# Kernel tuning notes

Measured on AMD Instinct MI355X. Metric: run time of the kernel, lower is better.

The kernel has to match this reference:

```python
import jax, jax.numpy as jnp
import numpy as np

B, L, D = 8, 2048, 512
H, P = 8, 4
C = D // H  # dim_per_head


def setup_inputs() -> dict:
    key = jax.random.key(0)
    ks = jax.random.split(key, 11)
    sc = lambda k, shape, s=0.02: jax.random.normal(k, shape, jnp.float32) * s
    return dict(
        query=jax.random.normal(ks[0], (B, L, D), jnp.float32),
        key_in=jax.random.normal(ks[1], (B, L, D), jnp.float32),
        value=jax.random.normal(ks[2], (B, L, D), jnp.float32),
        W_v=sc(ks[3], (D, D)), b_v=jnp.zeros((D,), jnp.float32),
        W_off=sc(ks[4], (D, H * P * 2), 0.01), b_off=sc(ks[5], (H * P * 2,), 0.2),
        W_aw=sc(ks[6], (D, H * P), 0.01), b_aw=jnp.zeros((H * P,), jnp.float32),
        W_out=sc(ks[7], (D, D)), b_out=jnp.zeros((D,), jnp.float32),
    )


def reference(query, key_in, value, W_v, b_v, W_off, b_off, W_aw, b_aw, W_out, b_out):
    # value projection
    v = value @ W_v + b_v                                        # (B,L,D)
    # sampling offsets and attention weights from the query
    off = (query @ W_off + b_off).reshape(B, L, H, P, 2)         # (B,L,H,P,2)
    aw = jax.nn.softmax((query @ W_aw + b_aw).reshape(B, L, H, P), axis=-1)
    # reference point for query i is (x=linspace[0]=0, y=linspace[i]) because
    # the torch code slices reference_points[:, :, :, :1, :]
    ref_y = jnp.linspace(0.0, 1.0, L, dtype=jnp.float32)
    loc_x = jnp.clip(off[..., 0], 0.0, 1.0)                      # ref_x = 0
    loc_y = jnp.clip(off[..., 1] + ref_y[None, :, None, None], 0.0, 1.0)
    # grid_sample, align_corners=False, input (BH, C, 1, L)
    ix = ((loc_x + 1.0) * L - 1.0) * 0.5                         # width coord in [ (L-1)/2, L-0.5 ]
    iy = loc_y * 0.5                                             # ((y+1)*1 - 1)/2
    ix0 = jnp.floor(ix)
    fx = ix - ix0
    iy0 = jnp.floor(iy)
    fy = iy - iy0
    # height dim has size 1: row iy0 valid iff ==0, row iy0+1 valid iff ==0 (zero padding)
    ywt = (1.0 - fy) * (iy0 == 0.0).astype(jnp.float32) + fy * ((iy0 + 1.0) == 0.0).astype(jnp.float32)
    i0 = ix0.astype(jnp.int32)
    i1 = i0 + 1

    perm = lambda a: a.transpose(0, 2, 1, 3)                     # (B,L,H,P) -> (B,H,L,P)
    i0p, i1p = perm(i0), perm(i1)
    vh = v.reshape(B, L, H, C).transpose(0, 2, 1, 3)             # (B,H,L,C)

    gather = jax.vmap(jax.vmap(lambda vm, ii: vm[ii]))           # (L,C),(L,P) -> (L,P,C)
    m0 = ((i0p >= 0) & (i0p < L)).astype(jnp.float32)[..., None]
    m1 = ((i1p >= 0) & (i1p < L)).astype(jnp.float32)[..., None]
    g0 = gather(vh, jnp.clip(i0p, 0, L - 1)) * m0                # (B,H,L,P,C)
    g1 = gather(vh, jnp.clip(i1p, 0, L - 1)) * m1

    fxp = perm(fx)[..., None]
    ywtp = perm(ywt)[..., None]
    samp = ywtp * ((1.0 - fxp) * g0 + fxp * g1)                  # (B,H,L,P,C)
    out = (samp * perm(aw)[..., None]).sum(axis=3)               # (B,H,L,C)
    out = out.transpose(0, 2, 1, 3).reshape(B, L, D)
    return out @ W_out + b_out
```

## Files before the change

### kernel.cpp

```cpp
#include <hip/hip_runtime.h>
#include <stdint.h>

#define PSZF (16384 * 96)

using short8  = __attribute__((ext_vector_type(8))) short;
using floatx4 = __attribute__((ext_vector_type(4))) float;

__device__ __forceinline__ unsigned short f2bf(float f) {
  union { float f; unsigned u; } v; v.f = f;
  unsigned r = v.u + 0x7fffu + ((v.u >> 16) & 1u);
  return (unsigned short)(r >> 16);
}
__device__ __forceinline__ float bf2f(unsigned short u) {
  union { unsigned u; float f; } v; v.u = ((unsigned)u) << 16; return v.f;
}

__device__ __forceinline__ void load_lds16(const void* g, void* l) {
  __builtin_amdgcn_global_load_lds(
      (const __attribute__((address_space(1))) unsigned int*)g,
      (__attribute__((address_space(3))) unsigned int*)l, 16, 0, 0);
}

__device__ __forceinline__ void store_val(float* p, float v) { *p = v; }
__device__ __forceinline__ void store_val(unsigned short* p, float v) { *p = f2bf(v); }

__global__ __launch_bounds__(256) void prep_all(const float* __restrict__ value,
                                                const float* __restrict__ W_v,
                                                const float* __restrict__ W_out,
                                                const float* __restrict__ Woff,
                                                const float* __restrict__ Waw,
                                                const float* __restrict__ boff,
                                                const float* __restrict__ baw,
                                                unsigned short* __restrict__ val_bf,
                                                unsigned short* __restrict__ Wv_t,
                                                unsigned short* __restrict__ Wo_t,
                                                unsigned short* __restrict__ Bhi,
                                                unsigned short* __restrict__ Blo,
                                                float* __restrict__ bcat) {
  int idx = blockIdx.x * 256 + threadIdx.x;
  if (idx < 2097152) {
    float4 v = ((const float4*)value)[idx];
    ushort4 o;
    o.x = f2bf(v.x); o.y = f2bf(v.y); o.z = f2bf(v.z); o.w = f2bf(v.w);
    ((ushort4*)val_bf)[idx] = o;
    return;
  }
  int t = idx - 2097152;
  if (t < 262144) {
    int n = t >> 9, k = t & 511;
    Wv_t[t] = f2bf(W_v[(k << 9) + n]);
    return;
  }
  t -= 262144;
  if (t < 262144) {
    int n = t >> 9, k = t & 511;
    Wo_t[t] = f2bf(W_out[(k << 9) + n]);
    return;
  }
  t -= 262144;
  if (t < 49152) {
    int n = t >> 9, k = t & 511;
    float w = (n < 64) ? Woff[(k << 6) + n] : Waw[(k << 5) + (n - 64)];
    unsigned short hi = f2bf(w);
    Bhi[t] = hi;
    Blo[t] = f2bf(w - bf2f(hi));
    return;
  }
  t -= 49152;
  if (t < 96) bcat[t] = (t < 64) ? boff[t] : baw[t - 64];
}

template <typename OutT>
__device__ __forceinline__ void gemm_body64(unsigned char* smem,
                                            const unsigned short* __restrict__ A,
                                            const unsigned short* __restrict__ Bt,
                                            const float* __restrict__ bias,
                                            OutT* __restrict__ C, int bx, int by) {
  unsigned short* lA = (unsigned short*)smem;
  unsigned short* lB = (unsigned short*)(smem + 16384);
  int tid  = threadIdx.x;
  int lane = tid & 63, wv = tid >> 6;
  int wm = wv & 1, wn = wv >> 1;
  int lrow = lane & 15, quad = lane >> 4;
  int rowBlk = by * 128, colBlk = bx * 128;

  const unsigned short* Ab = A + (size_t)rowBlk * 512;
  const unsigned short* Bb = Bt + (size_t)colBlk * 512;
  int r0 = tid >> 2;
  int c0 = (tid & 3) << 3;

  floatx4 acc[4][4];
#pragma unroll
  for (int i = 0; i < 4; i++)
#pragma unroll
    for (int j = 0; j < 4; j++) acc[i][j] = (floatx4){0.f, 0.f, 0.f, 0.f};

  for (int k0 = 0; k0 < 512; k0 += 64) {
    load_lds16(Ab + (size_t)r0 * 512 + k0 + c0,             lA + tid * 8);
    load_lds16(Ab + (size_t)(r0 + 64) * 512 + k0 + c0,      lA + 2048 + tid * 8);
    load_lds16(Bb + (size_t)r0 * 512 + k0 + c0,             lB + tid * 8);
    load_lds16(Bb + (size_t)(r0 + 64) * 512 + k0 + c0,      lB + 2048 + tid * 8);
    load_lds16(Ab + (size_t)r0 * 512 + k0 + 32 + c0,        lA + 4096 + tid * 8);
    load_lds16(Ab + (size_t)(r0 + 64) * 512 + k0 + 32 + c0, lA + 6144 + tid * 8);
    load_lds16(Bb + (size_t)r0 * 512 + k0 + 32 + c0,        lB + 4096 + tid * 8);
    load_lds16(Bb + (size_t)(r0 + 64) * 512 + k0 + 32 + c0, lB + 6144 + tid * 8);
    __syncthreads();

#pragma unroll
    for (int kc = 0; kc < 2; kc++) {
      short8 a[4], b[4];
#pragma unroll
      for (int mi = 0; mi < 4; mi++)
        a[mi] = *(const short8*)&lA[kc * 4096 + (wm * 64 + mi * 16 + lrow) * 32 + quad * 8];
#pragma unroll
      for (int ni = 0; ni < 4; ni++)
        b[ni] = *(const short8*)&lB[kc * 4096 + (wn * 64 + ni * 16 + lrow) * 32 + quad * 8];
#pragma unroll
      for (int mi = 0; mi < 4; mi++)
#pragma unroll
        for (int ni = 0; ni < 4; ni++)
          acc[mi][ni] = __builtin_amdgcn_mfma_f32_16x16x32_bf16(a[mi], b[ni], acc[mi][ni], 0, 0, 0);
    }
    __syncthreads();
  }

#pragma unroll
  for (int ni = 0; ni < 4; ni++) {
    int col = colBlk + wn * 64 + ni * 16 + lrow;
    float bv = bias[col];
#pragma unroll
    for (int mi = 0; mi < 4; mi++) {
      int row = rowBlk + wm * 64 + mi * 16 + quad * 4;
#pragma unroll
      for (int r = 0; r < 4; r++)
        store_val(&C[(size_t)(row + r) * 512 + col], acc[mi][ni][r] + bv);
    }
  }
}

__device__ __forceinline__ void swz512(int bid, int& bx, int& by) {
  int x = bid & 7, s = bid >> 3;
  by = (x << 4) | (s >> 2);
  bx = s & 3;
}

__device__ __forceinline__ void offaw_body(unsigned char* smem,
                                           const float* __restrict__ Q,
                                           const unsigned short* __restrict__ Bhi,
                                           const unsigned short* __restrict__ Blo,
                                           const float* __restrict__ bcat,
                                           float* __restrict__ P, int bid) {
  unsigned short* lAhi = (unsigned short*)smem;
  unsigned short* lAlo = (unsigned short*)(smem + 4096);
  unsigned short* lBhi = (unsigned short*)(smem + 8192);
  unsigned short* lBlo = (unsigned short*)(smem + 14336);
  int khalf = bid >> 8, row0 = (bid & 255) * 64, kbase = khalf << 8;
  int tid = threadIdx.x, lane = tid & 63, wv = tid >> 6;
  int wm = wv & 1, wn = wv >> 1, lrow = lane & 15, quad = lane >> 4;

  int ar = tid >> 2, ac = (tid & 3) << 3;
  const float* qp = Q + (size_t)(row0 + ar) * 512 + kbase + ac;

  floatx4 acc[2][3];
#pragma unroll
  for (int i = 0; i < 2; i++)
#pragma unroll
    for (int j = 0; j < 3; j++) acc[i][j] = (floatx4){0.f, 0.f, 0.f, 0.f};

  for (int k0 = 0; k0 < 256; k0 += 32) {
    float4 v0 = *(const float4*)(qp + k0);
    float4 v1 = *(const float4*)(qp + k0 + 4);
    float vv[8] = {v0.x, v0.y, v0.z, v0.w, v1.x, v1.y, v1.z, v1.w};
    short8 h8, l8;
#pragma unroll
    for (int e = 0; e < 8; e++) {
      union { float f; unsigned u; } t; t.f = vv[e];
      unsigned r = t.u + 0x7fffu + ((t.u >> 16) & 1u);
      h8[e] = (short)(r >> 16);
      union { unsigned u; float f; } hf; hf.u = r & 0xffff0000u;
      union { float f; unsigned u; } rb; rb.f = vv[e] - hf.f;
      l8[e] = (short)(rb.u >> 16);
    }
    *(short8*)&lAhi[tid * 8] = h8;
    *(short8*)&lAlo[tid * 8] = l8;
#pragma unroll
    for (int j = 0; j < 3; j++) {
      int widx = wv + (j << 2);
      const unsigned short* src = (widx < 6) ? Bhi : Blo;
      unsigned short* dst = (widx < 6) ? lBhi : lBlo;
      int c = (((widx < 6) ? widx : widx - 6) << 6) + lane;
      int n = c >> 2, cc = (c & 3) << 3;
      load_lds16(src + (size_t)n * 512 + kbase + k0 + cc, dst + c * 8);
    }
    __syncthreads();

    short8 ah[2], al[2], bh[3], bl[3];
#pragma unroll
    for (int mi = 0; mi < 2; mi++) {
      int r = (wm * 32 + mi * 16 + lrow) * 32 + quad * 8;
      ah[mi] = *(const short8*)&lAhi[r];
      al[mi] = *(const short8*)&lAlo[r];
    }
#pragma unroll
    for (int ni = 0; ni < 3; ni++) {
      int r = (wn * 48 + ni * 16 + lrow) * 32 + quad * 8;
      bh[ni] = *(const short8*)&lBhi[r];
      bl[ni] = *(const short8*)&lBlo[r];
    }
#pragma unroll
    for (int mi = 0; mi < 2; mi++)
#pragma unroll
      for (int ni = 0; ni < 3; ni++) {
        acc[mi][ni] = __builtin_amdgcn_mfma_f32_16x16x32_bf16(ah[mi], bh[ni], acc[mi][ni], 0, 0, 0);
        acc[mi][ni] = __builtin_amdgcn_mfma_f32_16x16x32_bf16(ah[mi], bl[ni], acc[mi][ni], 0, 0, 0);
        acc[mi][ni] = __builtin_amdgcn_mfma_f32_16x16x32_bf16(al[mi], bh[ni], acc[mi][ni], 0, 0, 0);
      }
    __syncthreads();
  }

  float* out = P + (size_t)khalf * PSZF;
#pragma unroll
  for (int ni = 0; ni < 3; ni++) {
    int col = wn * 48 + ni * 16 + lrow;
    float bv = (khalf == 0) ? bcat[col] : 0.0f;
#pragma unroll
    for (int mi = 0; mi < 2; mi++) {
      int row = row0 + wm * 32 + mi * 16 + quad * 4;
#pragma unroll
      for (int r = 0; r < 4; r++)
        out[(size_t)(row + r) * 96 + col] = acc[mi][ni][r] + bv;
    }
  }
}

__global__ __launch_bounds__(256) void mega_k1(const unsigned short* __restrict__ val_bf,
                                               const unsigned short* __restrict__ Wv_t,
                                               const float* __restrict__ b_v,
                                               unsigned short* __restrict__ v_bf,
                                               const float* __restrict__ query,
                                               const unsigned short* __restrict__ Bhi,
                                               const unsigned short* __restrict__ Blo,
                                               const float* __restrict__ bcat,
                                               float* __restrict__ offP) {
  __shared__ __align__(16) unsigned char smem[32768];
  int bid = blockIdx.x;
  if (bid < 512) {
    int bx, by; swz512(bid, bx, by);
    gemm_body64<unsigned short>(smem, val_bf, Wv_t, b_v, v_bf, bx, by);
  } else {
    offaw_body(smem, query, Bhi, Blo, bcat, offP, bid - 512);
  }
}

__global__ __launch_bounds__(256) void gemm2_k(const unsigned short* __restrict__ A,
                                               const unsigned short* __restrict__ Bt,
                                               const float* __restrict__ bias,
                                               float* __restrict__ C) {
  __shared__ __align__(16) unsigned char smem[32768];
  int bx, by; swz512(blockIdx.x, bx, by);
  gemm_body64<float>(smem, A, Bt, bias, C, bx, by);
}

__global__ __launch_bounds__(256) void sample_kernel(const float* __restrict__ P,
                                                     const unsigned short* __restrict__ v,
                                                     unsigned short* __restrict__ attn) {
  int tid = threadIdx.x;
  int rr = tid >> 5, hp = tid & 31;
  int row = blockIdx.x * 8 + rr;
  int l = row & 2047;
  __shared__ float s_w0[8][32], s_w1[8][32];
  __shared__ int s_i0[8][32], s_i1[8][32];
  {
    int base = row * 96;
    float lg = P[base + 64 + hp] + P[PSZF + base + 64 + hp];
    float mx = fmaxf(lg, __shfl_xor(lg, 1));
    mx = fmaxf(mx, __shfl_xor(mx, 2));
    float e = __expf(lg - mx);
    float s = e + __shfl_xor(e, 1);
    s = s + __shfl_xor(s, 2);
    float aw = e / s;

    float ox = P[base + 2 * hp] + P[PSZF + base + 2 * hp];
    float oy = P[base + 2 * hp + 1] + P[PSZF + base + 2 * hp + 1];
    float refy = (float)l * (1.0f / 2047.0f);
    float lx = fminf(fmaxf(ox, 0.0f), 1.0f);
    float ly = fminf(fmaxf(oy + refy, 0.0f), 1.0f);
    float ix = ((lx + 1.0f) * 2048.0f - 1.0f) * 0.5f;
    float ywt = 1.0f - ly * 0.5f;
    float ix0 = floorf(ix);
    float fx = ix - ix0;
    int i0 = (int)ix0;
    int i1 = i0 + 1;
    s_w0[rr][hp] = aw * ywt * (1.0f - fx);
    s_w1[rr][hp] = (i1 < 2048) ? (aw * ywt * fx) : 0.0f;
    s_i0[rr][hp] = i0;
    s_i1[rr][hp] = (i1 < 2048) ? i1 : 2047;
  }
  __syncthreads();

  int b = (blockIdx.x * 8) >> 11;
  int h = tid >> 5, c = (tid & 31) << 1;
  const unsigned short* vhc = v + ((size_t)(b << 11)) * 512 + h * 64 + c;
#pragma unroll
  for (int r8 = 0; r8 < 8; r8++) {
    int row2 = blockIdx.x * 8 + r8;
    float ax = 0.0f, ay = 0.0f;
#pragma unroll
    for (int p = 0; p < 4; p++) {
      int t = (h << 2) + p;
      unsigned g0 = *(const unsigned*)(vhc + ((size_t)s_i0[r8][t] << 9));
      unsigned g1 = *(const unsigned*)(vhc + ((size_t)s_i1[r8][t] << 9));
      float w0 = s_w0[r8][t], w1 = s_w1[r8][t];
      ax += w0 * bf2f((unsigned short)g0) + w1 * bf2f((unsigned short)g1);
      ay += w0 * bf2f((unsigned short)(g0 >> 16)) + w1 * bf2f((unsigned short)(g1 >> 16));
    }
    unsigned packed = (unsigned)f2bf(ax) | ((unsigned)f2bf(ay) << 16);
    *(unsigned*)(attn + (size_t)row2 * 512 + h * 64 + c) = packed;
  }
}

extern "C" void kernel_launch(void* const* d_in, const int* in_sizes, int n_in,
                              void* d_out, int out_size, void* d_ws, size_t ws_size,
                              hipStream_t stream) {
  (void)in_sizes; (void)n_in; (void)out_size; (void)ws_size;
  const float* query = (const float*)d_in[0];
  const float* value = (const float*)d_in[2];
  const float* W_v   = (const float*)d_in[3];
  const float* b_v   = (const float*)d_in[4];
  const float* W_off = (const float*)d_in[5];
  const float* b_off = (const float*)d_in[6];
  const float* W_aw  = (const float*)d_in[7];
  const float* b_aw  = (const float*)d_in[8];
  const float* W_out = (const float*)d_in[9];
  const float* b_out = (const float*)d_in[10];
  float* out = (float*)d_out;

  char* ws = (char*)d_ws;
  const size_t MB = 1ull << 20;
  unsigned short* val_bf = (unsigned short*)(ws);
  unsigned short* attn   = val_bf;
  unsigned short* v_bf   = (unsigned short*)(ws + 16 * MB);
  float* offP            = (float*)(ws + 32 * MB);
  unsigned short* Wv_t   = (unsigned short*)(ws + 48 * MB);
  unsigned short* Wo_t   = (unsigned short*)(ws + 48 * MB + 524288);
  unsigned short* Bhi    = (unsigned short*)(ws + 49 * MB);
  unsigned short* Blo    = (unsigned short*)(ws + 49 * MB + 98304);
  float* bcat            = (float*)(ws + 49 * MB + 196608);

  prep_all<<<10433, 256, 0, stream>>>(value, W_v, W_out, W_off, W_aw, b_off, b_aw,
                                      val_bf, Wv_t, Wo_t, Bhi, Blo, bcat);
  mega_k1<<<1024, 256, 0, stream>>>(val_bf, Wv_t, b_v, v_bf, query, Bhi, Blo, bcat, offP);
  sample_kernel<<<2048, 256, 0, stream>>>(offP, v_bf, attn);
  gemm2_k<<<512, 256, 0, stream>>>(attn, Wo_t, b_out, out);
}
```

Before: 192.7 us.

## Fuse deformable sampling with output projection GEMM via LDS-staged tile

Merges the sampling kernel and the output-projection GEMM into one kernel. Each block computes a 32-row bf16 attention tile in shared memory, then multiplies it by W_out with MFMA, reading the B operand straight from global memory. This drops the global round trip of the attention intermediate and one launch. In exchange there are only 512 blocks, each using about 48KB of shared memory, and W_out is re-read per block without LDS staging, so occupancy and B-operand bandwidth may suffer.

Measured after the change: 227.6 us. +18.1%, slower.

```diff
diff --git a/kernel.cpp b/kernel.cpp
--- a/kernel.cpp
+++ b/kernel.cpp
@@ -252,25 +252,26 @@
   }
 }
 
-__global__ __launch_bounds__(256) void gemm2_k(const unsigned short* __restrict__ A,
-                                               const unsigned short* __restrict__ Bt,
-                                               const float* __restrict__ bias,
-                                               float* __restrict__ C) {
-  __shared__ __align__(16) unsigned char smem[32768];
-  int bx, by; swz512(blockIdx.x, bx, by);
-  gemm_body64<float>(smem, A, Bt, bias, C, bx, by);
-}
-
-__global__ __launch_bounds__(256) void sample_kernel(const float* __restrict__ P,
-                                                     const unsigned short* __restrict__ v,
-                                                     unsigned short* __restrict__ attn) {
+__global__ __launch_bounds__(256) void sample_out_kernel(const float* __restrict__ P,
+                                                         const unsigned short* __restrict__ v,
+                                                         const unsigned short* __restrict__ Wo,
+                                                         const float* __restrict__ bias,
+                                                         float* __restrict__ out) {
+  __shared__ float s_w0[32][32], s_w1[32][32];
+  __shared__ int s_i0[32][32], s_i1[32][32];
+  __shared__ __align__(16) unsigned short s_attn[16384];
+
   int tid = threadIdx.x;
+  int bid = blockIdx.x;
+  int sw = ((bid & 7) << 6) + (bid >> 3);
+  int row0 = sw << 5;
+
   int rr = tid >> 5, hp = tid & 31;
-  int row = blockIdx.x * 8 + rr;
-  int l = row & 2047;
-  __shared__ float s_w0[8][32], s_w1[8][32];
-  __shared__ int s_i0[8][32], s_i1[8][32];
-  {
+#pragma unroll
+  for (int it = 0; it < 4; ++it) {
+    int rl = (it << 3) + rr;
+    int row = row0 + rl;
+    int l = row & 2047;
     int base = row * 96;
     float lg = P[base + 64 + hp] + P[PSZF + base + 64 + hp];
     float mx = fmaxf(lg, __shfl_xor(lg, 1));
@@ -291,22 +292,23 @@
     float fx = ix - ix0;
     int i0 = (int)ix0;
     int i1 = i0 + 1;
-    s_w0[rr][hp] = aw * ywt * (1.0f - fx);
-    s_w1[rr][hp] = (i1 < 2048) ? (aw * ywt * fx) : 0.0f;
-    s_i0[rr][hp] = i0;
-    s_i1[rr][hp] = (i1 < 2048) ? i1 : 2047;
+    s_w0[rl][hp] = aw * ywt * (1.0f - fx);
+    s_w1[rl][hp] = (i1 < 2048) ? (aw * ywt * fx) : 0.0f;
+    s_i0[rl][hp] = i0;
+    s_i1[rl][hp] = (i1 < 2048) ? i1 : 2047;
   }
   __syncthreads();
 
-  int b = (blockIdx.x * 8) >> 11;
+  int b = row0 >> 11;
   int h = tid >> 5, c = (tid & 31) << 1;
   const unsigned short* vhc = v + ((size_t)(b << 11)) * 512 + h * 64 + c;
-#pragma unroll
-  for (int r8 = 0; r8 < 8; r8++) {
-    int row2 = blockIdx.x * 8 + r8;
+  int ch = h * 64 + c;
+  char* sa = (char*)s_attn + ((ch >> 5) << 11) + ((c & 31) << 1);
+#pragma unroll 4
+  for (int r8 = 0; r8 < 32; ++r8) {
     float ax = 0.0f, ay = 0.0f;
 #pragma unroll
-    for (int p = 0; p < 4; p++) {
+    for (int p = 0; p < 4; ++p) {
       int t = (h << 2) + p;
       unsigned g0 = *(const unsigned*)(vhc + ((size_t)s_i0[r8][t] << 9));
       unsigned g1 = *(const unsigned*)(vhc + ((size_t)s_i1[r8][t] << 9));
@@ -314,8 +316,46 @@
       ax += w0 * bf2f((unsigned short)g0) + w1 * bf2f((unsigned short)g1);
       ay += w0 * bf2f((unsigned short)(g0 >> 16)) + w1 * bf2f((unsigned short)(g1 >> 16));
     }
-    unsigned packed = (unsigned)f2bf(ax) | ((unsigned)f2bf(ay) << 16);
-    *(unsigned*)(attn + (size_t)row2 * 512 + h * 64 + c) = packed;
+    *(unsigned*)(sa + (r8 << 6)) = (unsigned)f2bf(ax) | ((unsigned)f2bf(ay) << 16);
+  }
+  __syncthreads();
+
+  int lane = tid & 63, wv = tid >> 6;
+  int lrow = lane & 15, quad = lane >> 4;
+  floatx4 acc[2][8];
+#pragma unroll
+  for (int mi = 0; mi < 2; ++mi)
+#pragma unroll
+    for (int ni = 0; ni < 8; ++ni) acc[mi][ni] = (floatx4){0.f, 0.f, 0.f, 0.f};
+
+  const unsigned short* Bb = Wo + ((size_t)wv << 7) * 512;
+#pragma unroll 2
+  for (int k0 = 0; k0 < 512; k0 += 32) {
+    short8 a[2];
+#pragma unroll
+    for (int mi = 0; mi < 2; ++mi)
+      a[mi] = *(const short8*)((const char*)s_attn +
+                               ((k0 >> 5) << 11) + (((mi << 4) + lrow) << 6) + (quad << 4));
+#pragma unroll
+    for (int ni = 0; ni < 8; ++ni) {
+      short8 bfrag = *(const short8*)&Bb[(size_t)((ni << 4) + lrow) * 512 + k0 + (quad << 3)];
+#pragma unroll
+      for (int mi = 0; mi < 2; ++mi)
+        acc[mi][ni] = __builtin_amdgcn_mfma_f32_16x16x32_bf16(a[mi], bfrag, acc[mi][ni], 0, 0, 0);
+    }
+  }
+
+#pragma unroll
+  for (int ni = 0; ni < 8; ++ni) {
+    int col = (wv << 7) + (ni << 4) + lrow;
+    float bv = bias[col];
+#pragma unroll
+    for (int mi = 0; mi < 2; ++mi) {
+      int row = row0 + (mi << 4) + (quad << 2);
+#pragma unroll
+      for (int r = 0; r < 4; ++r)
+        out[(size_t)(row + r) * 512 + col] = acc[mi][ni][r] + bv;
+    }
   }
 }
 
@@ -338,7 +378,6 @@
   char* ws = (char*)d_ws;
   const size_t MB = 1ull << 20;
   unsigned short* val_bf = (unsigned short*)(ws);
-  unsigned short* attn   = val_bf;
   unsigned short* v_bf   = (unsigned short*)(ws + 16 * MB);
   float* offP            = (float*)(ws + 32 * MB);
   unsigned short* Wv_t   = (unsigned short*)(ws + 48 * MB);
@@ -350,6 +389,5 @@
   prep_all<<<10433, 256, 0, stream>>>(value, W_v, W_out, W_off, W_aw, b_off, b_aw,
                                       val_bf, Wv_t, Wo_t, Bhi, Blo, bcat);
   mega_k1<<<1024, 256, 0, stream>>>(val_bf, Wv_t, b_v, v_bf, query, Bhi, Blo, bcat, offP);
-  sample_kernel<<<2048, 256, 0, stream>>>(offP, v_bf, attn);
-  gemm2_k<<<512, 256, 0, stream>>>(attn, Wo_t, b_out, out);
-}
+  sample_out_kernel<<<512, 256, 0, stream>>>(offP, v_bf, Wo_t, b_out, out);
+}
```

## Double-buffer LDS tiles in the bf16 GEMM k-loop to overlap loads with MFMA

Applied to the files above, without the earlier changes.

The 128x128 GEMM body now steps k in chunks of 32 instead of 64, using two LDS buffers. The global-to-LDS loads for the next chunk are issued right after the barrier, while the MFMAs for the current chunk run. This replaces the old load, sync, compute, sync pattern, so global load latency can hide behind compute and each step needs one barrier instead of two. In exchange the loop runs twice as many steps, and correctness depends on the barrier waiting for the asynchronous LDS loads to finish.

Result: no change. 193.1 us (+0.2%).

```diff
diff --git a/kernel.cpp b/kernel.cpp
--- a/kernel.cpp
+++ b/kernel.cpp
@@ -76,8 +76,8 @@
                                             const unsigned short* __restrict__ Bt,
                                             const float* __restrict__ bias,
                                             OutT* __restrict__ C, int bx, int by) {
-  unsigned short* lA = (unsigned short*)smem;
-  unsigned short* lB = (unsigned short*)(smem + 16384);
+  unsigned short* lAb = (unsigned short*)smem;
+  unsigned short* lBb = (unsigned short*)(smem + 16384);
   int tid  = threadIdx.x;
   int lane = tid & 63, wv = tid >> 6;
   int wm = wv & 1, wn = wv >> 1;
@@ -95,33 +95,38 @@
 #pragma unroll
     for (int j = 0; j < 4; j++) acc[i][j] = (floatx4){0.f, 0.f, 0.f, 0.f};
 
-  for (int k0 = 0; k0 < 512; k0 += 64) {
-    load_lds16(Ab + (size_t)r0 * 512 + k0 + c0,             lA + tid * 8);
-    load_lds16(Ab + (size_t)(r0 + 64) * 512 + k0 + c0,      lA + 2048 + tid * 8);
-    load_lds16(Bb + (size_t)r0 * 512 + k0 + c0,             lB + tid * 8);
-    load_lds16(Bb + (size_t)(r0 + 64) * 512 + k0 + c0,      lB + 2048 + tid * 8);
-    load_lds16(Ab + (size_t)r0 * 512 + k0 + 32 + c0,        lA + 4096 + tid * 8);
-    load_lds16(Ab + (size_t)(r0 + 64) * 512 + k0 + 32 + c0, lA + 6144 + tid * 8);
-    load_lds16(Bb + (size_t)r0 * 512 + k0 + 32 + c0,        lB + 4096 + tid * 8);
-    load_lds16(Bb + (size_t)(r0 + 64) * 512 + k0 + 32 + c0, lB + 6144 + tid * 8);
+  {
+    load_lds16(Ab + (size_t)r0 * 512 + c0,        lAb + tid * 8);
+    load_lds16(Ab + (size_t)(r0 + 64) * 512 + c0, lAb + 2048 + tid * 8);
+    load_lds16(Bb + (size_t)r0 * 512 + c0,        lBb + tid * 8);
+    load_lds16(Bb + (size_t)(r0 + 64) * 512 + c0, lBb + 2048 + tid * 8);
+  }
+
+#pragma unroll
+  for (int t = 0; t < 16; ++t) {
+    int cur = t & 1;
     __syncthreads();
-
-#pragma unroll
-    for (int kc = 0; kc < 2; kc++) {
-      short8 a[4], b[4];
-#pragma unroll
-      for (int mi = 0; mi < 4; mi++)
-        a[mi] = *(const short8*)&lA[kc * 4096 + (wm * 64 + mi * 16 + lrow) * 32 + quad * 8];
+    if (t < 15) {
+      int nb = (cur ^ 1) * 4096;
+      int kk = (t + 1) * 32;
+      load_lds16(Ab + (size_t)r0 * 512 + kk + c0,        lAb + nb + tid * 8);
+      load_lds16(Ab + (size_t)(r0 + 64) * 512 + kk + c0, lAb + nb + 2048 + tid * 8);
+      load_lds16(Bb + (size_t)r0 * 512 + kk + c0,        lBb + nb + tid * 8);
+      load_lds16(Bb + (size_t)(r0 + 64) * 512 + kk + c0, lBb + nb + 2048 + tid * 8);
+    }
+    int cb = cur * 4096;
+    short8 a[4], b[4];
+#pragma unroll
+    for (int mi = 0; mi < 4; mi++)
+      a[mi] = *(const short8*)&lAb[cb + (wm * 64 + mi * 16 + lrow) * 32 + quad * 8];
+#pragma unroll
+    for (int ni = 0; ni < 4; ni++)
+      b[ni] = *(const short8*)&lBb[cb + (wn * 64 + ni * 16 + lrow) * 32 + quad * 8];
+#pragma unroll
+    for (int mi = 0; mi < 4; mi++)
 #pragma unroll
       for (int ni = 0; ni < 4; ni++)
-        b[ni] = *(const short8*)&lB[kc * 4096 + (wn * 64 + ni * 16 + lrow) * 32 + quad * 8];
-#pragma unroll
-      for (int mi = 0; mi < 4; mi++)
-#pragma unroll
-        for (int ni = 0; ni < 4; ni++)
-          acc[mi][ni] = __builtin_amdgcn_mfma_f32_16x16x32_bf16(a[mi], b[ni], acc[mi][ni], 0, 0, 0);
-    }
-    __syncthreads();
+        acc[mi][ni] = __builtin_amdgcn_mfma_f32_16x16x32_bf16(a[mi], b[ni], acc[mi][ni], 0, 0, 0);
   }
 
 #pragma unroll
```
